# Kernel tuning notes

Measured on AMD Instinct MI355X. Metric: run time of the kernel, lower is better.

The kernel has to match this reference:

```python
import jax, jax.numpy as jnp
import numpy as np

NUM_EVENT_TYPES = 100000
EMBED_DIM = 16
SEQ_LEN = 4194304
TAU = 0.1


def setup_inputs() -> dict:
    key = jax.random.key(0)
    k1, k2, k3, k4, k5 = jax.random.split(key, 5)
    event_trace = jax.random.randint(k1, (SEQ_LEN,), 0, NUM_EVENT_TYPES, dtype=jnp.int32)
    embed_table = jax.random.normal(k2, (NUM_EVENT_TYPES, EMBED_DIM), dtype=jnp.float32)
    w_attn = jax.random.normal(k3, (EMBED_DIM,), dtype=jnp.float32) * (1.0 / np.sqrt(EMBED_DIM))
    b_attn = jax.random.normal(k4, (), dtype=jnp.float32) * 0.01
    causality_logits = jnp.zeros((NUM_EVENT_TYPES,), dtype=jnp.float32)
    return {
        "event_trace": event_trace,
        "is_crash": 1,
        "embed_table": embed_table,
        "w_attn": w_attn,
        "b_attn": b_attn,
        "causality_logits": causality_logits,
    }


def reference(event_trace, is_crash, embed_table, w_attn, b_attn, causality_logits):
    # gather embeddings: [S, D]
    embeds = embed_table[event_trace]
    # attn projection to scalar logit per position: [S]
    attn_logits = embeds @ w_attn + b_attn
    # softmax over the whole trace
    attn_weights = jax.nn.softmax(attn_logits / TAU, axis=0)
    # scatter-add attention mass per event type (segment sum): [T]
    type_attention = jax.ops.segment_sum(attn_weights, event_trace,
                                         num_segments=NUM_EVENT_TYPES)
    # type_attention is zero for types absent from the trace, so summing over
    # all types equals the original's sum over unique(event_trace).
    causality = jax.nn.sigmoid(causality_logits)
    explained = jnp.clip(jnp.sum(type_attention * causality), 0.0, 1.0)
    contradiction = jnp.where(jnp.asarray(is_crash) > 0.5,
                              jax.nn.relu(1.0 - explained),
                              jax.nn.relu(explained))
    return contradiction
```

## Files before the change

kernel.cpp:

```cpp
#include <hip/hip_runtime.h>
#include <math.h>

namespace {

constexpr float kInvTau = 10.0f;
constexpr int   kBlock  = 256;
constexpr int   kGrid   = 2048;
constexpr float kNegBig = -1e30f;

__global__ void pc_kernel(const float* __restrict__ table,
                          const float* __restrict__ w,
                          const float* __restrict__ b,
                          const float* __restrict__ cl,
                          float2* __restrict__ pc, int T) {
    int t = blockIdx.x * blockDim.x + threadIdx.x;
    if (t >= T) return;
    const float4* row = reinterpret_cast<const float4*>(table) + (size_t)t * 4;
    const float4* wv  = reinterpret_cast<const float4*>(w);
    float4 r0 = row[0], r1 = row[1], r2 = row[2], r3 = row[3];
    float4 w0 = wv[0],  w1 = wv[1],  w2 = wv[2],  w3 = wv[3];
    float dot = r0.x*w0.x + r0.y*w0.y + r0.z*w0.z + r0.w*w0.w
              + r1.x*w1.x + r1.y*w1.y + r1.z*w1.z + r1.w*w1.w
              + r2.x*w2.x + r2.y*w2.y + r2.z*w2.z + r2.w*w2.w
              + r3.x*w3.x + r3.y*w3.y + r3.z*w3.z + r3.w*w3.w;
    float p = (dot + b[0]) * kInvTau;
    float c = 1.0f / (1.0f + __expf(-cl[t]));
    pc[t] = make_float2(p, c);
}

__device__ __forceinline__ void merge_state(float& m, float& s, float& t,
                                            float m2, float s2, float t2) {
    float nm = fmaxf(m, m2);
    float r1 = __expf(m  - nm);
    float r2 = __expf(m2 - nm);
    s = s * r1 + s2 * r2;
    t = t * r1 + t2 * r2;
    m = nm;
}

__device__ __forceinline__ void block_reduce(float& m, float& s, float& t) {
    #pragma unroll
    for (int off = 1; off < 64; off <<= 1) {
        float m2 = __shfl_xor(m, off);
        float s2 = __shfl_xor(s, off);
        float t2 = __shfl_xor(t, off);
        merge_state(m, s, t, m2, s2, t2);
    }
    __shared__ float sm[4], ss[4], st[4];
    int lane = threadIdx.x & 63;
    int wave = threadIdx.x >> 6;
    if (lane == 0) { sm[wave] = m; ss[wave] = s; st[wave] = t; }
    __syncthreads();
    if (threadIdx.x == 0) {
        int nw = blockDim.x >> 6;
        for (int i = 1; i < nw; ++i)
            merge_state(m, s, t, sm[i], ss[i], st[i]);
    }
}

__global__ __launch_bounds__(kBlock)
void pass_kernel(const int* __restrict__ trace, int S,
                 const float2* __restrict__ pc,
                 float4* __restrict__ blk) {
    float m = kNegBig, s = 0.f, t = 0.f;
    int tid    = blockIdx.x * blockDim.x + threadIdx.x;
    int stride = gridDim.x * blockDim.x;

    const int4* trace4 = reinterpret_cast<const int4*>(trace);
    int S4 = S >> 2;
    for (int i = tid; i < S4; i += stride) {
        int4 v = trace4[i];
        float2 a0 = pc[v.x], a1 = pc[v.y], a2 = pc[v.z], a3 = pc[v.w];
        float lm = fmaxf(fmaxf(a0.x, a1.x), fmaxf(a2.x, a3.x));
        if (lm > m) {
            float r = __expf(m - lm);
            s *= r; t *= r; m = lm;
        }
        float e0 = __expf(a0.x - m);
        float e1 = __expf(a1.x - m);
        float e2 = __expf(a2.x - m);
        float e3 = __expf(a3.x - m);
        s += (e0 + e1) + (e2 + e3);
        t += (e0 * a0.y + e1 * a1.y) + (e2 * a2.y + e3 * a3.y);
    }
    for (int i = (S4 << 2) + tid; i < S; i += stride) {
        float2 a = pc[trace[i]];
        if (a.x > m) { float r = __expf(m - a.x); s *= r; t *= r; m = a.x; }
        float e = __expf(a.x - m);
        s += e; t += e * a.y;
    }

    block_reduce(m, s, t);
    if (threadIdx.x == 0) blk[blockIdx.x] = make_float4(m, s, t, 0.f);
}

__global__ void final_kernel(const float4* __restrict__ blk, int nblk,
                             const int* __restrict__ is_crash,
                             float* __restrict__ out) {
    float m = kNegBig, s = 0.f, t = 0.f;
    for (int i = threadIdx.x; i < nblk; i += blockDim.x) {
        float4 b = blk[i];
        merge_state(m, s, t, b.x, b.y, b.z);
    }
    block_reduce(m, s, t);
    if (threadIdx.x == 0) {
        float explained = (s > 0.f) ? (t / s) : 0.f;
        explained = fminf(fmaxf(explained, 0.f), 1.f);
        float contradiction = (is_crash[0] > 0)
            ? fmaxf(1.0f - explained, 0.f)
            : fmaxf(explained, 0.f);
        out[0] = contradiction;
    }
}

}

extern "C" void kernel_launch(void* const* d_in, const int* in_sizes, int n_in,
                              void* d_out, int out_size, void* d_ws, size_t ws_size,
                              hipStream_t stream) {
    const int*   trace = (const int*)  d_in[0];
    const int*   crash = (const int*)  d_in[1];
    const float* table = (const float*)d_in[2];
    const float* w     = (const float*)d_in[3];
    const float* b     = (const float*)d_in[4];
    const float* cl    = (const float*)d_in[5];
    float*       out   = (float*)d_out;

    const int S = in_sizes[0];
    const int T = in_sizes[5];

    float2* pc  = (float2*)d_ws;
    float4* blk = (float4*)((char*)d_ws + (size_t)T * sizeof(float2));

    int gridA = (T + kBlock - 1) / kBlock;
    pc_kernel<<<gridA, kBlock, 0, stream>>>(table, w, b, cl, pc, T);
    pass_kernel<<<kGrid, kBlock, 0, stream>>>(trace, S, pc, blk);
    final_kernel<<<1, kBlock, 0, stream>>>(blk, kGrid, crash, out);
}
```

Before: 33.40 us.

## Precompute per-type exp weights using global max over table instead of online softmax

Takes the softmax max over all event types rather than over the trace, found with an atomicMax on order-preserving uint keys, and precomputes exp(p-M) and exp(p-M)*sigmoid per type in a new kernel. The main pass then gathers and sums two floats per element without any exp or rescaling. Trace loads are nontemporal and partial sums use split accumulators. Using a max over types that may be absent from the trace is still exact for the ratio t/s, but it adds two launches and a memset.

```diff
diff --git a/kernel.cpp b/kernel.cpp
--- a/kernel.cpp
+++ b/kernel.cpp
@@ -5,105 +5,125 @@
 
 constexpr float kInvTau = 10.0f;
 constexpr int   kBlock  = 256;
-constexpr int   kGrid   = 2048;
-constexpr float kNegBig = -1e30f;
+constexpr int   kGridH  = 2048;
 
-__global__ void pc_kernel(const float* __restrict__ table,
-                          const float* __restrict__ w,
-                          const float* __restrict__ b,
-                          const float* __restrict__ cl,
-                          float2* __restrict__ pc, int T) {
-    int t = blockIdx.x * blockDim.x + threadIdx.x;
-    if (t >= T) return;
-    const float4* row = reinterpret_cast<const float4*>(table) + (size_t)t * 4;
-    const float4* wv  = reinterpret_cast<const float4*>(w);
-    float4 r0 = row[0], r1 = row[1], r2 = row[2], r3 = row[3];
-    float4 w0 = wv[0],  w1 = wv[1],  w2 = wv[2],  w3 = wv[3];
-    float dot = r0.x*w0.x + r0.y*w0.y + r0.z*w0.z + r0.w*w0.w
-              + r1.x*w1.x + r1.y*w1.y + r1.z*w1.z + r1.w*w1.w
-              + r2.x*w2.x + r2.y*w2.y + r2.z*w2.z + r2.w*w2.w
-              + r3.x*w3.x + r3.y*w3.y + r3.z*w3.z + r3.w*w3.w;
-    float p = (dot + b[0]) * kInvTau;
-    float c = 1.0f / (1.0f + __expf(-cl[t]));
-    pc[t] = make_float2(p, c);
+typedef int v4i __attribute__((ext_vector_type(4)));
+
+__device__ __forceinline__ unsigned ord_of(float f) {
+    unsigned b = __float_as_uint(f);
+    return (b & 0x80000000u) ? ~b : (b | 0x80000000u);
+}
+__device__ __forceinline__ float float_of_ord(unsigned o) {
+    unsigned b = (o & 0x80000000u) ? (o ^ 0x80000000u) : ~o;
+    return __uint_as_float(b);
 }
 
-__device__ __forceinline__ void merge_state(float& m, float& s, float& t,
-                                            float m2, float s2, float t2) {
-    float nm = fmaxf(m, m2);
-    float r1 = __expf(m  - nm);
-    float r2 = __expf(m2 - nm);
-    s = s * r1 + s2 * r2;
-    t = t * r1 + t2 * r2;
-    m = nm;
-}
-
-__device__ __forceinline__ void block_reduce(float& m, float& s, float& t) {
+__global__ __launch_bounds__(kBlock)
+void prep_kernel(const float* __restrict__ table,
+                 const float* __restrict__ w,
+                 const float* __restrict__ b,
+                 const float* __restrict__ cl,
+                 float2* __restrict__ pc,
+                 unsigned* __restrict__ maxo, int T) {
+    int t = blockIdx.x * blockDim.x + threadIdx.x;
+    float p = -1e30f;
+    if (t < T) {
+        const float4* row = reinterpret_cast<const float4*>(table) + (size_t)t * 4;
+        const float4* wv  = reinterpret_cast<const float4*>(w);
+        float4 r0 = row[0], r1 = row[1], r2 = row[2], r3 = row[3];
+        float4 w0 = wv[0],  w1 = wv[1],  w2 = wv[2],  w3 = wv[3];
+        float dot = r0.x*w0.x + r0.y*w0.y + r0.z*w0.z + r0.w*w0.w
+                  + r1.x*w1.x + r1.y*w1.y + r1.z*w1.z + r1.w*w1.w
+                  + r2.x*w2.x + r2.y*w2.y + r2.z*w2.z + r2.w*w2.w
+                  + r3.x*w3.x + r3.y*w3.y + r3.z*w3.z + r3.w*w3.w;
+        p = (dot + b[0]) * kInvTau;
+        float c = 1.0f / (1.0f + __expf(-cl[t]));
+        pc[t] = make_float2(p, c);
+    }
+    float pm = p;
     #pragma unroll
-    for (int off = 1; off < 64; off <<= 1) {
-        float m2 = __shfl_xor(m, off);
-        float s2 = __shfl_xor(s, off);
-        float t2 = __shfl_xor(t, off);
-        merge_state(m, s, t, m2, s2, t2);
-    }
-    __shared__ float sm[4], ss[4], st[4];
-    int lane = threadIdx.x & 63;
-    int wave = threadIdx.x >> 6;
-    if (lane == 0) { sm[wave] = m; ss[wave] = s; st[wave] = t; }
+    for (int off = 1; off < 64; off <<= 1)
+        pm = fmaxf(pm, __shfl_xor(pm, off));
+    __shared__ float wm[4];
+    int lane = threadIdx.x & 63, wave = threadIdx.x >> 6;
+    if (lane == 0) wm[wave] = pm;
     __syncthreads();
     if (threadIdx.x == 0) {
-        int nw = blockDim.x >> 6;
-        for (int i = 1; i < nw; ++i)
-            merge_state(m, s, t, sm[i], ss[i], st[i]);
+        float bm = fmaxf(fmaxf(wm[0], wm[1]), fmaxf(wm[2], wm[3]));
+        atomicMax(maxo, ord_of(bm));
     }
 }
 
 __global__ __launch_bounds__(kBlock)
+void ebgen_kernel(const float2* __restrict__ pc,
+                  const unsigned* __restrict__ maxo,
+                  float2* __restrict__ g, int T) {
+    int t = blockIdx.x * blockDim.x + threadIdx.x;
+    if (t >= T) return;
+    float M = float_of_ord(*maxo);
+    float2 a = pc[t];
+    float eb = __expf(a.x - M);
+    g[t] = make_float2(eb, eb * a.y);
+}
+
+__global__ __launch_bounds__(kBlock)
 void pass_kernel(const int* __restrict__ trace, int S,
-                 const float2* __restrict__ pc,
-                 float4* __restrict__ blk) {
-    float m = kNegBig, s = 0.f, t = 0.f;
+                 const float2* __restrict__ g,
+                 float2* __restrict__ blk) {
+    float s0 = 0.f, s1 = 0.f, t0 = 0.f, t1 = 0.f;
     int tid    = blockIdx.x * blockDim.x + threadIdx.x;
     int stride = gridDim.x * blockDim.x;
-
-    const int4* trace4 = reinterpret_cast<const int4*>(trace);
+    const v4i* trace4 = reinterpret_cast<const v4i*>(trace);
     int S4 = S >> 2;
+    #pragma unroll 2
     for (int i = tid; i < S4; i += stride) {
-        int4 v = trace4[i];
-        float2 a0 = pc[v.x], a1 = pc[v.y], a2 = pc[v.z], a3 = pc[v.w];
-        float lm = fmaxf(fmaxf(a0.x, a1.x), fmaxf(a2.x, a3.x));
-        if (lm > m) {
-            float r = __expf(m - lm);
-            s *= r; t *= r; m = lm;
-        }
-        float e0 = __expf(a0.x - m);
-        float e1 = __expf(a1.x - m);
-        float e2 = __expf(a2.x - m);
-        float e3 = __expf(a3.x - m);
-        s += (e0 + e1) + (e2 + e3);
-        t += (e0 * a0.y + e1 * a1.y) + (e2 * a2.y + e3 * a3.y);
+        v4i v = __builtin_nontemporal_load(&trace4[i]);
+        float2 a0 = g[v.x], a1 = g[v.y], a2 = g[v.z], a3 = g[v.w];
+        s0 += a0.x + a2.x;  t0 += a0.y + a2.y;
+        s1 += a1.x + a3.x;  t1 += a1.y + a3.y;
     }
     for (int i = (S4 << 2) + tid; i < S; i += stride) {
-        float2 a = pc[trace[i]];
-        if (a.x > m) { float r = __expf(m - a.x); s *= r; t *= r; m = a.x; }
-        float e = __expf(a.x - m);
-        s += e; t += e * a.y;
+        float2 a = g[trace[i]];
+        s0 += a.x; t0 += a.y;
     }
-
-    block_reduce(m, s, t);
-    if (threadIdx.x == 0) blk[blockIdx.x] = make_float4(m, s, t, 0.f);
+    float s = s0 + s1, t = t0 + t1;
+    #pragma unroll
+    for (int off = 1; off < 64; off <<= 1) {
+        s += __shfl_xor(s, off);
+        t += __shfl_xor(t, off);
+    }
+    __shared__ float ws_[4], wt_[4];
+    int lane = threadIdx.x & 63, wave = threadIdx.x >> 6;
+    if (lane == 0) { ws_[wave] = s; wt_[wave] = t; }
+    __syncthreads();
+    if (threadIdx.x == 0) {
+        s = ws_[0] + ws_[1] + ws_[2] + ws_[3];
+        t = wt_[0] + wt_[1] + wt_[2] + wt_[3];
+        blk[blockIdx.x] = make_float2(s, t);
+    }
 }
 
-__global__ void final_kernel(const float4* __restrict__ blk, int nblk,
-                             const int* __restrict__ is_crash,
-                             float* __restrict__ out) {
-    float m = kNegBig, s = 0.f, t = 0.f;
+__global__ __launch_bounds__(kBlock)
+void final_kernel(const float2* __restrict__ blk, int nblk,
+                  const int* __restrict__ is_crash,
+                  float* __restrict__ out) {
+    float s = 0.f, t = 0.f;
     for (int i = threadIdx.x; i < nblk; i += blockDim.x) {
-        float4 b = blk[i];
-        merge_state(m, s, t, b.x, b.y, b.z);
+        float2 b = blk[i];
+        s += b.x; t += b.y;
     }
-    block_reduce(m, s, t);
+    #pragma unroll
+    for (int off = 1; off < 64; off <<= 1) {
+        s += __shfl_xor(s, off);
+        t += __shfl_xor(t, off);
+    }
+    __shared__ float ws_[4], wt_[4];
+    int lane = threadIdx.x & 63, wave = threadIdx.x >> 6;
+    if (lane == 0) { ws_[wave] = s; wt_[wave] = t; }
+    __syncthreads();
     if (threadIdx.x == 0) {
+        s = ws_[0] + ws_[1] + ws_[2] + ws_[3];
+        t = wt_[0] + wt_[1] + wt_[2] + wt_[3];
         float explained = (s > 0.f) ? (t / s) : 0.f;
         explained = fminf(fmaxf(explained, 0.f), 1.f);
         float contradiction = (is_crash[0] > 0)
@@ -129,11 +149,17 @@
     const int S = in_sizes[0];
     const int T = in_sizes[5];
 
-    float2* pc  = (float2*)d_ws;
-    float4* blk = (float4*)((char*)d_ws + (size_t)T * sizeof(float2));
+    char* p = (char*)d_ws;
+    float2*   pc   = (float2*)p;   p += (size_t)T * sizeof(float2);
+    float2*   g    = (float2*)p;   p += (size_t)T * sizeof(float2);
+    float2*   blk  = (float2*)p;   p += (size_t)kGridH * sizeof(float2);
+    unsigned* maxo = (unsigned*)p;
 
-    int gridA = (T + kBlock - 1) / kBlock;
-    pc_kernel<<<gridA, kBlock, 0, stream>>>(table, w, b, cl, pc, T);
-    pass_kernel<<<kGrid, kBlock, 0, stream>>>(trace, S, pc, blk);
-    final_kernel<<<1, kBlock, 0, stream>>>(blk, kGrid, crash, out);
+    hipMemsetAsync(maxo, 0, sizeof(unsigned), stream);
+
+    int gridT = (T + kBlock - 1) / kBlock;
+    prep_kernel <<<gridT, kBlock, 0, stream>>>(table, w, b, cl, pc, maxo, T);
+    ebgen_kernel<<<gridT, kBlock, 0, stream>>>(pc, maxo, g, T);
+    pass_kernel <<<kGridH, kBlock, 0, stream>>>(trace, S, g, blk);
+    final_kernel<<<1, kBlock, 0, stream>>>(blk, kGridH, crash, out);
 }
```

Result: slower. 40.86 us (+22.3%).
